# Performance work log

Measured on AMD Instinct MI355X. Metric: run time of the kernel, lower is better.

The kernel has to match this reference:

```python
import jax, jax.numpy as jnp
import numpy as np

N = 20000      # nodes
E = 320000     # edges (avg degree 16)
IN = 128
HID = 64
CLS = 32
H0, H1, H2 = 4, 4, 6
SLOPE = 0.2


def _lin(key, fan_in, fan_out):
    kw, kb = jax.random.split(key)
    s = 1.0 / np.sqrt(fan_in)
    W = jax.random.uniform(kw, (fan_in, fan_out), minval=-s, maxval=s, dtype=jnp.float32)
    b = jax.random.uniform(kb, (fan_out,), minval=-s, maxval=s, dtype=jnp.float32)
    return W, b


def setup_inputs() -> dict:
    key = jax.random.key(0)
    ks = jax.random.split(key, 16)
    x = jax.random.normal(ks[0], (N, IN), dtype=jnp.float32)
    src = jax.random.randint(ks[1], (E,), 0, N)
    dst = jax.random.randint(ks[2], (E,), 0, N)
    W0s, b0s = _lin(ks[3], IN, H0 * HID)
    W0d, b0d = _lin(ks[4], IN, H0 * HID)
    a0 = jax.random.normal(ks[5], (H0, HID), dtype=jnp.float32) * 0.05
    d1 = H0 * HID  # 256, flattened hidden width
    W1s, b1s = _lin(ks[6], d1, H1 * HID)
    W1d, b1d = _lin(ks[7], d1, H1 * HID)
    a1 = jax.random.normal(ks[8], (H1, HID), dtype=jnp.float32) * 0.05
    W2s, b2s = _lin(ks[9], d1, H2 * CLS)
    W2d, b2d = _lin(ks[10], d1, H2 * CLS)
    a2 = jax.random.normal(ks[11], (H2, CLS), dtype=jnp.float32) * 0.05
    Wr2, br2 = _lin(ks[12], d1, H2 * CLS)  # residual projection (256 != 192)
    return dict(x=x, src=src, dst=dst,
                W0s=W0s, b0s=b0s, W0d=W0d, b0d=b0d, a0=a0,
                W1s=W1s, b1s=b1s, W1d=W1d, b1d=b1d, a1=a1,
                W2s=W2s, b2s=b2s, W2d=W2d, b2d=b2d, a2=a2,
                Wr2=Wr2, br2=br2)


def _gatv2_layer(x, src, dst, Ws, bs, Wd, bd, attn, heads, dim, res, act):
    n = x.shape[0]
    feat_src = (x @ Ws + bs).reshape(n, heads, dim)
    feat_dst = (x @ Wd + bd).reshape(n, heads, dim)
    # GATv2 edge scores: a^T LeakyReLU(W_l h_u + W_r h_v)
    e = jax.nn.leaky_relu(feat_src[src] + feat_dst[dst], SLOPE)  # [E,H,D]
    logits = jnp.einsum('ehd,hd->eh', e, attn)                    # [E,H]
    # numerically-stable edge softmax over incoming edges per destination
    m = jax.ops.segment_max(logits, dst, num_segments=n)
    m = jnp.where(jnp.isfinite(m), m, 0.0)
    ex = jnp.exp(logits - m[dst])
    denom = jax.ops.segment_sum(ex, dst, num_segments=n)
    alpha = ex / denom[dst]                                        # [E,H]
    out = jax.ops.segment_sum(feat_src[src] * alpha[:, :, None], dst, num_segments=n)
    if res == 'id':
        out = out + x.reshape(n, heads, dim)
    elif res is not None:
        Wr, br = res
        out = out + (x @ Wr + br).reshape(n, heads, dim)
    if act:
        out = jax.nn.elu(out)
    return out  # [n, heads, dim]


def reference(x, src, dst,
              W0s, b0s, W0d, b0d, a0,
              W1s, b1s, W1d, b1d, a1,
              W2s, b2s, W2d, b2d, a2,
              Wr2, br2):
    h = _gatv2_layer(x, src, dst, W0s, b0s, W0d, b0d, a0, H0, HID, None, True)
    h = h.reshape(N, H0 * HID)
    h = _gatv2_layer(h, src, dst, W1s, b1s, W1d, b1d, a1, H1, HID, 'id', True)
    h = h.reshape(N, H1 * HID)
    out = _gatv2_layer(h, src, dst, W2s, b2s, W2d, b2d, a2, H2, CLS, (Wr2, br2), False)
    return out.mean(axis=1)  # [N, num_classes]
```

## Files before the change

### kernel.cpp

```cpp
#include <hip/hip_runtime.h>
#include <hip/hip_bf16.h>
#include <float.h>
#include <math.h>

#define NN 20000
#define EE 320000
#define IN_DIM 128
#define SLOPE_ 0.2f
#define DEG_CAP 64

typedef __attribute__((ext_vector_type(4))) float f32x4;
typedef _Float16 f16;
typedef __attribute__((ext_vector_type(2))) _Float16 f16x2;
typedef __attribute__((ext_vector_type(4))) _Float16 f16x4;
typedef __attribute__((ext_vector_type(8))) _Float16 f16x8;
typedef unsigned short ushort;

__device__ inline void prep_elem(const float* __restrict__ Wa, const float* __restrict__ ba, int na,
                                 const float* __restrict__ Wb, const float* __restrict__ bb, int nb,
                                 const float* __restrict__ Wc, const float* __restrict__ bc, int nc,
                                 int K, f16* __restrict__ Wt, float* __restrict__ bias_cat, int idx) {
    int n = idx / K;
    int k = idx - n * K;
    const float* W; const float* b; int nl; int ncols;
    if (n < na) { W = Wa; b = ba; nl = n; ncols = na; }
    else if (n < na + nb) { W = Wb; b = bb; nl = n - na; ncols = nb; }
    else { W = Wc; b = bc; nl = n - na - nb; ncols = nc; }
    Wt[(size_t)n * K + k] = (f16)W[(size_t)k * ncols + nl];
    if (k == 0) bias_cat[n] = b[nl];
}

#define SEG0 (512 * 128)
#define SEG1 (512 * 256)
#define SEG2 (576 * 256)
#define SEG3 (NN * IN_DIM / 4)
#define SEG4 (EE)
__global__ void prep_all(const float* __restrict__ W0s, const float* __restrict__ b0s,
                         const float* __restrict__ W0d, const float* __restrict__ b0d,
                         const float* __restrict__ W1s, const float* __restrict__ b1s,
                         const float* __restrict__ W1d, const float* __restrict__ b1d,
                         const float* __restrict__ W2s, const float* __restrict__ b2s,
                         const float* __restrict__ W2d, const float* __restrict__ b2d,
                         const float* __restrict__ Wr2, const float* __restrict__ br2,
                         const float* __restrict__ x,
                         const int* __restrict__ src, const int* __restrict__ dst,
                         f16* __restrict__ Wt0, float* __restrict__ bias0,
                         f16* __restrict__ Wt1, float* __restrict__ bias1,
                         f16* __restrict__ Wt2, float* __restrict__ bias2,
                         f16* __restrict__ A, unsigned int* __restrict__ deg,
                         int* __restrict__ csr_src) {
    int idx = blockIdx.x * 256 + threadIdx.x;
    if (idx < SEG0) {
        prep_elem(W0s, b0s, 256, W0d, b0d, 256, nullptr, nullptr, 0, 128, Wt0, bias0, idx);
    } else if ((idx -= SEG0) < SEG1) {
        prep_elem(W1s, b1s, 256, W1d, b1d, 256, nullptr, nullptr, 0, 256, Wt1, bias1, idx);
    } else if ((idx -= SEG1) < SEG2) {
        prep_elem(W2s, b2s, 192, W2d, b2d, 192, Wr2, br2, 192, 256, Wt2, bias2, idx);
    } else if ((idx -= SEG2) < SEG3) {
        float4 v = ((const float4*)x)[idx];
        f16x4 o = {(f16)v.x, (f16)v.y, (f16)v.z, (f16)v.w};
        ((f16x4*)A)[idx] = o;
    } else if ((idx -= SEG3) < SEG4) {
        int d = dst[idx];
        unsigned int pos = atomicAdd(&deg[d], 1u);
        csr_src[(unsigned)d * DEG_CAP + pos] = src[idx];
    }
}

__global__ __launch_bounds__(256) void gemm_mfma_f16(
        const f16* __restrict__ A, const f16* __restrict__ Wt,
        const float* __restrict__ bias,
        f16* __restrict__ F0, f16* __restrict__ F1, float* __restrict__ F2,
        int b1, int b2, int M, int K, int S, int gx, int gy) {
    __shared__ f16 Bs[64 * 256];
    __shared__ f16 Cs[4][32 * 66];

    const int bid = blockIdx.x;
    const int p = bid & 7;
    const int q = bid >> 3;
    const int bn_i = q % gx;
    const int bm_i = (q / gx) * 8 + p;
    if (bm_i >= gy) return;
    const int bm = bm_i * 256;
    const int bn = bn_i * 64;

    const int tid = threadIdx.x;
    const int wave = tid >> 6;
    const int lane = tid & 63;
    const int m16 = lane & 15;
    const int quad = lane >> 4;

    {
        const int n = tid >> 2;
        const int q0 = tid & 3;
        for (int j = 0; j * 32 < K; ++j) {
            int k0 = j * 32 + q0 * 8;
            f16x8 v = *(const f16x8*)(Wt + (size_t)(bn + n) * K + k0);
            int chunk = (j * 4 + (n >> 4)) * 64 + q0 * 16 + (n & 15);
            *(f16x8*)&Bs[chunk * 8] = v;
        }
    }
    __syncthreads();

    const int rb0 = bm + wave * 64;
    f32x4 acc[2][2][4];
    #pragma unroll
    for (int mi = 0; mi < 2; ++mi)
        #pragma unroll
        for (int mt = 0; mt < 2; ++mt)
            #pragma unroll
            for (int nt = 0; nt < 4; ++nt) acc[mi][mt][nt] = (f32x4){0.f, 0.f, 0.f, 0.f};

    int ar[2][2];
    #pragma unroll
    for (int mi = 0; mi < 2; ++mi)
        #pragma unroll
        for (int mt = 0; mt < 2; ++mt) {
            int row = rb0 + mi * 32 + mt * 16 + m16;
            ar[mi][mt] = row < M ? row : M - 1;
        }

    #pragma unroll 2
    for (int k0 = 0; k0 < K; k0 += 32) {
        f16x8 bs[4];
        #pragma unroll
        for (int nt = 0; nt < 4; ++nt)
            bs[nt] = *(const f16x8*)&Bs[(((k0 >> 5) * 4 + nt) * 64 + lane) * 8];
        #pragma unroll
        for (int mi = 0; mi < 2; ++mi) {
            f16x8 ah[2];
            #pragma unroll
            for (int mt = 0; mt < 2; ++mt)
                ah[mt] = *(const f16x8*)(A + (size_t)ar[mi][mt] * K + k0 + quad * 8);
            #pragma unroll
            for (int nt = 0; nt < 4; ++nt)
                #pragma unroll
                for (int mt = 0; mt < 2; ++mt)
                    acc[mi][mt][nt] = __builtin_amdgcn_mfma_f32_16x16x32_f16(ah[mt], bs[nt], acc[mi][mt][nt], 0, 0, 0);
        }
    }

    #pragma unroll
    for (int mi = 0; mi < 2; ++mi) {
        const int rbase = rb0 + mi * 32;
        if (bn < b2) {
            f16* __restrict__ Fb;
            int cs, cb;
            if (bn >= b1) { Fb = F1; cb = bn - b1; cs = b2 - b1; }
            else          { Fb = F0; cb = bn;      cs = b1; }
            f16* cw = &Cs[wave][0];
            #pragma unroll
            for (int nt = 0; nt < 4; ++nt) {
                float bv = bias[bn + nt * 16 + m16];
                #pragma unroll
                for (int mt = 0; mt < 2; ++mt)
                    #pragma unroll
                    for (int r = 0; r < 4; ++r) {
                        int row = mt * 16 + quad * 4 + r;
                        cw[row * 66 + nt * 16 + m16] = (f16)(acc[mi][mt][nt][r] + bv);
                    }
            }
            int lrow = lane >> 1;
            int lcol = (lane & 1) * 32;
            int grow = rbase + lrow;
            if (grow < M) {
                #pragma unroll
                for (int j = 0; j < 4; ++j) {
                    f16x8 v = *(f16x8*)&cw[lrow * 66 + lcol + j * 8];
                    *(f16x8*)&Fb[(size_t)grow * cs + cb + lcol + j * 8] = v;
                }
            }
        } else {
            int cs = S - b2;
            #pragma unroll
            for (int nt = 0; nt < 4; ++nt) {
                int col = bn - b2 + nt * 16 + m16;
                float bv = bias[bn + nt * 16 + m16];
                #pragma unroll
                for (int mt = 0; mt < 2; ++mt)
                    #pragma unroll
                    for (int r = 0; r < 4; ++r) {
                        int row = rbase + mt * 16 + quad * 4 + r;
                        if (row < M) F2[(size_t)row * cs + col] = acc[mi][mt][nt][r] + bv;
                    }
            }
        }
    }
}

#define AGG_STEP4(U0)                                                         \
    _Pragma("unroll")                                                         \
    for (int uu = 0; uu < 4; ++uu) {                                          \
        const int u = (U0) + uu;                                              \
        const f16x8 cur = buf[u];                                             \
        buf[u] = *(const f16x8*)&fsb[(unsigned)cidx[u] * HD + off];           \
        cidx[u] = csr_src[min(jj0 + b + 16 + u, last)];                       \
        float p = 0.f;                                                        \
        _Pragma("unroll")                                                     \
        for (int i = 0; i < 4; ++i) {                                         \
            f16x2 cp = (f16x2){cur[2 * i], cur[2 * i + 1]};                   \
            f16x2 xp = cp + fdp[i];                                           \
            unsigned xu = __builtin_bit_cast(unsigned, xp) & 0x7FFF7FFFu;     \
            f16x2 xa = __builtin_bit_cast(f16x2, xu);                         \
            p = __builtin_amdgcn_fdot2(xp, a6p[i], p, false);                 \
            p = __builtin_amdgcn_fdot2(xa, a4p[i], p, false);                 \
        }                                                                     \
        _Pragma("unroll")                                                     \
        for (int o = 1; o < GSZ; o <<= 1) p += __shfl_xor(p, o, 64);          \
        float w = (b + u < deg) ? __expf(p) : 0.f;                            \
        lh += w;                                                              \
        _Pragma("unroll")                                                     \
        for (int d = 0; d < 8; ++d) acc[d] += w * (float)cur[d];              \
    }

template <int HD, int D, bool HAS_RES, bool DO_ELU, int OUT_MODE>
__global__ __launch_bounds__(256) void gat_node_aggregate(
        const f16* __restrict__ fsb, const f16* __restrict__ fdb,
        const float* __restrict__ attn,
        const unsigned int* __restrict__ degv,
        const int* __restrict__ csr_src,
        const float* __restrict__ resid, int RS,
        float* __restrict__ outF, f16* __restrict__ outA) {
    constexpr int LANES = HD / 8;
    constexpr int GSZ = D / 8;
    __shared__ float red[(OUT_MODE == 2) ? 8 : 1][(OUT_MODE == 2) ? HD : 1];

    const int wave = threadIdx.x >> 6;
    const int lane = threadIdx.x & 63;
    const int half = lane >> 5;
    const int ln = lane & 31;
    const int t = blockIdx.x * 8 + wave * 2 + half;
    const bool active = (ln < LANES);
    const unsigned off = active ? 8u * ln : 0u;

    f16x2 fdp[4], a6p[4], a4p[4];
    if (active) {
        f16x8 dv = *(const f16x8*)&fdb[(unsigned)t * HD + off];
        float4 aA = *(const float4*)&attn[off];
        float4 aB = *(const float4*)&attn[off + 4];
        float av[8] = {aA.x, aA.y, aA.z, aA.w, aB.x, aB.y, aB.z, aB.w};
        #pragma unroll
        for (int i = 0; i < 4; ++i) {
            fdp[i] = (f16x2){dv[2 * i], dv[2 * i + 1]};
            a6p[i] = (f16x2){(f16)(0.6f * av[2 * i]), (f16)(0.6f * av[2 * i + 1])};
            a4p[i] = (f16x2){(f16)(0.4f * av[2 * i]), (f16)(0.4f * av[2 * i + 1])};
        }
    } else {
        #pragma unroll
        for (int i = 0; i < 4; ++i) {
            fdp[i] = (f16x2){0, 0};
            a6p[i] = (f16x2){0, 0};
            a4p[i] = (f16x2){0, 0};
        }
    }

    const int jj0 = t * DEG_CAP;
    const int deg = (int)degv[t];
    const int last = jj0 + deg - 1;
    const int degO = __shfl_xor(deg, 32, 64);
    const int mdeg = max(deg, degO);

    float acc[8];
    #pragma unroll
    for (int d = 0; d < 8; ++d) acc[d] = 0.f;
    float lh = 0.f;

    f16x8 buf[8];
    int cidx[8];
    #pragma unroll
    for (int u = 0; u < 8; ++u) {
        int e0 = max(min(jj0 + u, last), 0);
        buf[u] = *(const f16x8*)&fsb[(unsigned)csr_src[e0] * HD + off];
        cidx[u] = csr_src[max(min(jj0 + 8 + u, last), 0)];
    }

    for (int b = 0; b < mdeg; b += 8) {
        AGG_STEP4(0)
        if (b + 4 < mdeg) {
            AGG_STEP4(4)
        }
    }

    float inv = (lh > 0.f) ? 1.f / lh : 0.f;
    float vout[8];
    #pragma unroll
    for (int d = 0; d < 8; ++d) vout[d] = acc[d] * inv;
    if (HAS_RES && active) {
        float4 rA = *(const float4*)&resid[(unsigned)t * RS + off];
        float4 rB = *(const float4*)&resid[(unsigned)t * RS + off + 4];
        vout[0] += rA.x; vout[1] += rA.y; vout[2] += rA.z; vout[3] += rA.w;
        vout[4] += rB.x; vout[5] += rB.y; vout[6] += rB.z; vout[7] += rB.w;
    }
    if (DO_ELU) {
        #pragma unroll
        for (int d = 0; d < 8; ++d) vout[d] = vout[d] > 0.f ? vout[d] : expm1f(vout[d]);
    }

    if (OUT_MODE == 2) {
        const int nib = wave * 2 + half;
        if (active) {
            *(float4*)&red[nib][off] = make_float4(vout[0], vout[1], vout[2], vout[3]);
            *(float4*)&red[nib][off + 4] = make_float4(vout[4], vout[5], vout[6], vout[7]);
        }
        __syncthreads();
        int node = threadIdx.x >> 5;
        int col = threadIdx.x & 31;
        float ssum = 0.f;
        #pragma unroll
        for (int h = 0; h < 6; ++h) ssum += red[node][h * 32 + col];
        outF[(unsigned)(blockIdx.x * 8 + node) * 32 + col] = ssum * (1.f / 6.f);
    } else if (active) {
        f16x8 av;
        #pragma unroll
        for (int d = 0; d < 8; ++d) av[d] = (f16)vout[d];
        *(f16x8*)&outA[(unsigned)t * HD + off] = av;
        if (OUT_MODE == 0) {
            *(float4*)&outF[(unsigned)t * HD + off] = make_float4(vout[0], vout[1], vout[2], vout[3]);
            *(float4*)&outF[(unsigned)t * HD + off + 4] = make_float4(vout[4], vout[5], vout[6], vout[7]);
        }
    }
}

extern "C" void kernel_launch(void* const* d_in, const int* in_sizes, int n_in,
                              void* d_out, int out_size, void* d_ws, size_t ws_size,
                              hipStream_t stream) {
    const float* x   = (const float*)d_in[0];
    const int*   src = (const int*)d_in[1];
    const int*   dst = (const int*)d_in[2];
    const float* W0s = (const float*)d_in[3];
    const float* b0s = (const float*)d_in[4];
    const float* W0d = (const float*)d_in[5];
    const float* b0d = (const float*)d_in[6];
    const float* a0  = (const float*)d_in[7];
    const float* W1s = (const float*)d_in[8];
    const float* b1s = (const float*)d_in[9];
    const float* W1d = (const float*)d_in[10];
    const float* b1d = (const float*)d_in[11];
    const float* a1  = (const float*)d_in[12];
    const float* W2s = (const float*)d_in[13];
    const float* b2s = (const float*)d_in[14];
    const float* W2d = (const float*)d_in[15];
    const float* b2d = (const float*)d_in[16];
    const float* a2  = (const float*)d_in[17];
    const float* Wr2 = (const float*)d_in[18];
    const float* br2 = (const float*)d_in[19];

    f16* FsH = (f16*)d_ws;
    f16* FdH = FsH + (size_t)NN * 256;
    f16* A   = FdH + (size_t)NN * 256;
    float* O0 = (float*)(A + (size_t)NN * 256);
    f16* Wt0 = (f16*)(O0 + (size_t)NN * 256);
    f16* Wt1 = Wt0 + 512 * 128;
    f16* Wt2 = Wt1 + 512 * 256;
    float* bias0 = (float*)(Wt2 + 576 * 256);
    float* bias1 = bias0 + 512;
    float* bias2 = bias1 + 512;
    unsigned int* deg = (unsigned int*)(bias2 + 576);
    int* csr_src      = (int*)(deg + NN);

    hipMemsetAsync(deg, 0, (size_t)NN * 4 + (size_t)NN * DEG_CAP * 4, stream);

    {
        int total = SEG0 + SEG1 + SEG2 + SEG3 + SEG4;
        prep_all<<<(total + 255) / 256, 256, 0, stream>>>(
            W0s, b0s, W0d, b0d, W1s, b1s, W1d, b1d, W2s, b2s, W2d, b2d, Wr2, br2, x,
            src, dst, Wt0, bias0, Wt1, bias1, Wt2, bias2, A, deg, csr_src);
    }

    const int gy = (NN + 255) / 256;
    const int gy8 = ((gy + 7) / 8) * 8;
    const int nagg = NN / 8;

    gemm_mfma_f16<<<gy8 * 8, 256, 0, stream>>>(A, Wt0, bias0,
                                               FsH, FdH, nullptr, 256, 512, NN, 128, 512, 8, gy);
    gat_node_aggregate<256, 64, false, true, 0><<<nagg, 256, 0, stream>>>(
        FsH, FdH, a0, deg, csr_src, nullptr, 0, O0, A);

    gemm_mfma_f16<<<gy8 * 8, 256, 0, stream>>>(A, Wt1, bias1,
                                               FsH, FdH, nullptr, 256, 512, NN, 256, 512, 8, gy);
    gat_node_aggregate<256, 64, true, true, 1><<<nagg, 256, 0, stream>>>(
        FsH, FdH, a1, deg, csr_src, O0, 256, nullptr, A);

    gemm_mfma_f16<<<gy8 * 9, 256, 0, stream>>>(A, Wt2, bias2,
                                               FsH, FdH, O0, 192, 384, NN, 256, 576, 9, gy);
    gat_node_aggregate<192, 32, true, false, 2><<<nagg, 256, 0, stream>>>(
        FsH, FdH, a2, deg, csr_src, O0, 192, (float*)d_out, nullptr);
}
```

Measured before the change: 285.3 us.

## Fuse all GAT stages into one persistent cooperative kernel with grid syncs

Replaces the memset plus seven separate launches with a single cooperative persistent kernel of 768 blocks. Prep, CSR build, the three GEMMs and the three aggregations run as grid-strided stages separated by grid.sync(). The aim is to remove launch gaps and the memset of the full CSR buffer; only the degree array is zeroed now, and CSR writes are clamped to the cap. In exchange the kernel carries grid barrier overhead, lower occupancy from launch bounds of 3 blocks, and grid-strided loops whose work may balance less well than the per-kernel grids did. A fallback multi-kernel path runs if the cooperative launch fails.

```diff
diff --git a/kernel.cpp b/kernel.cpp
--- a/kernel.cpp
+++ b/kernel.cpp
@@ -1,25 +1,44 @@
 #include <hip/hip_runtime.h>
-#include <hip/hip_bf16.h>
+#include <hip/hip_cooperative_groups.h>
 #include <float.h>
 #include <math.h>
+
+namespace cg = cooperative_groups;
 
 #define NN 20000
 #define EE 320000
 #define IN_DIM 128
-#define SLOPE_ 0.2f
 #define DEG_CAP 64
+#define TPB 256
+#define COOP_GRID 768
 
 typedef __attribute__((ext_vector_type(4))) float f32x4;
 typedef _Float16 f16;
 typedef __attribute__((ext_vector_type(2))) _Float16 f16x2;
 typedef __attribute__((ext_vector_type(4))) _Float16 f16x4;
 typedef __attribute__((ext_vector_type(8))) _Float16 f16x8;
-typedef unsigned short ushort;
-
-__device__ inline void prep_elem(const float* __restrict__ Wa, const float* __restrict__ ba, int na,
-                                 const float* __restrict__ Wb, const float* __restrict__ bb, int nb,
-                                 const float* __restrict__ Wc, const float* __restrict__ bc, int nc,
-                                 int K, f16* __restrict__ Wt, float* __restrict__ bias_cat, int idx) {
+
+#define SEG0 (512 * 128)
+#define SEG1 (512 * 256)
+#define SEG2 (576 * 256)
+#define SEG3 (NN * IN_DIM / 4)
+#define SEGZ_TOT (SEG0 + SEG1 + SEG2 + SEG3 + NN)
+#define FB_TOT (SEG0 + SEG1 + SEG2 + SEG3 + EE)
+
+struct GatArgs {
+    const float *x; const int *src; const int *dst;
+    const float *W0s, *b0s, *W0d, *b0d, *a0;
+    const float *W1s, *b1s, *W1d, *b1d, *a1;
+    const float *W2s, *b2s, *W2d, *b2d, *a2, *Wr2, *br2;
+    f16 *FsH, *FdH, *A; float *O0;
+    f16 *Wt0, *Wt1, *Wt2; float *bias0, *bias1, *bias2;
+    unsigned *deg; int *csr; float *out;
+};
+
+__device__ __forceinline__ void prep_elem(const float* __restrict__ Wa, const float* __restrict__ ba, int na,
+                                          const float* __restrict__ Wb, const float* __restrict__ bb, int nb,
+                                          const float* __restrict__ Wc, const float* __restrict__ bc, int nc,
+                                          int K, f16* __restrict__ Wt, float* __restrict__ bias_cat, int idx) {
     int n = idx / K;
     int k = idx - n * K;
     const float* W; const float* b; int nl; int ncols;
@@ -30,159 +49,138 @@
     if (k == 0) bias_cat[n] = b[nl];
 }
 
-#define SEG0 (512 * 128)
-#define SEG1 (512 * 256)
-#define SEG2 (576 * 256)
-#define SEG3 (NN * IN_DIM / 4)
-#define SEG4 (EE)
-__global__ void prep_all(const float* __restrict__ W0s, const float* __restrict__ b0s,
-                         const float* __restrict__ W0d, const float* __restrict__ b0d,
-                         const float* __restrict__ W1s, const float* __restrict__ b1s,
-                         const float* __restrict__ W1d, const float* __restrict__ b1d,
-                         const float* __restrict__ W2s, const float* __restrict__ b2s,
-                         const float* __restrict__ W2d, const float* __restrict__ b2d,
-                         const float* __restrict__ Wr2, const float* __restrict__ br2,
-                         const float* __restrict__ x,
-                         const int* __restrict__ src, const int* __restrict__ dst,
-                         f16* __restrict__ Wt0, float* __restrict__ bias0,
-                         f16* __restrict__ Wt1, float* __restrict__ bias1,
-                         f16* __restrict__ Wt2, float* __restrict__ bias2,
-                         f16* __restrict__ A, unsigned int* __restrict__ deg,
-                         int* __restrict__ csr_src) {
-    int idx = blockIdx.x * 256 + threadIdx.x;
+__device__ __forceinline__ bool prep_item(const GatArgs& g, int idx) {
     if (idx < SEG0) {
-        prep_elem(W0s, b0s, 256, W0d, b0d, 256, nullptr, nullptr, 0, 128, Wt0, bias0, idx);
+        prep_elem(g.W0s, g.b0s, 256, g.W0d, g.b0d, 256, nullptr, nullptr, 0, 128, g.Wt0, g.bias0, idx);
     } else if ((idx -= SEG0) < SEG1) {
-        prep_elem(W1s, b1s, 256, W1d, b1d, 256, nullptr, nullptr, 0, 256, Wt1, bias1, idx);
+        prep_elem(g.W1s, g.b1s, 256, g.W1d, g.b1d, 256, nullptr, nullptr, 0, 256, g.Wt1, g.bias1, idx);
     } else if ((idx -= SEG1) < SEG2) {
-        prep_elem(W2s, b2s, 192, W2d, b2d, 192, Wr2, br2, 192, 256, Wt2, bias2, idx);
+        prep_elem(g.W2s, g.b2s, 192, g.W2d, g.b2d, 192, g.Wr2, g.br2, 192, 256, g.Wt2, g.bias2, idx);
     } else if ((idx -= SEG2) < SEG3) {
-        float4 v = ((const float4*)x)[idx];
+        float4 v = ((const float4*)g.x)[idx];
         f16x4 o = {(f16)v.x, (f16)v.y, (f16)v.z, (f16)v.w};
-        ((f16x4*)A)[idx] = o;
-    } else if ((idx -= SEG3) < SEG4) {
-        int d = dst[idx];
-        unsigned int pos = atomicAdd(&deg[d], 1u);
-        csr_src[(unsigned)d * DEG_CAP + pos] = src[idx];
-    }
-}
-
-__global__ __launch_bounds__(256) void gemm_mfma_f16(
+        ((f16x4*)g.A)[idx] = o;
+    } else return false;
+    return true;
+}
+
+__device__ __forceinline__ void gemm_stage(
         const f16* __restrict__ A, const f16* __restrict__ Wt,
         const float* __restrict__ bias,
         f16* __restrict__ F0, f16* __restrict__ F1, float* __restrict__ F2,
-        int b1, int b2, int M, int K, int S, int gx, int gy) {
-    __shared__ f16 Bs[64 * 256];
-    __shared__ f16 Cs[4][32 * 66];
-
-    const int bid = blockIdx.x;
-    const int p = bid & 7;
-    const int q = bid >> 3;
-    const int bn_i = q % gx;
-    const int bm_i = (q / gx) * 8 + p;
-    if (bm_i >= gy) return;
-    const int bm = bm_i * 256;
-    const int bn = bn_i * 64;
-
+        int b1, int b2, int M, int K, int S, int gx, int gy, int gy8,
+        f16* Bs, f16* Cs, int vb0, int vstride) {
+    const int ntiles = gy8 * gx;
     const int tid = threadIdx.x;
     const int wave = tid >> 6;
     const int lane = tid & 63;
     const int m16 = lane & 15;
     const int quad = lane >> 4;
 
-    {
-        const int n = tid >> 2;
-        const int q0 = tid & 3;
-        for (int j = 0; j * 32 < K; ++j) {
-            int k0 = j * 32 + q0 * 8;
-            f16x8 v = *(const f16x8*)(Wt + (size_t)(bn + n) * K + k0);
-            int chunk = (j * 4 + (n >> 4)) * 64 + q0 * 16 + (n & 15);
-            *(f16x8*)&Bs[chunk * 8] = v;
-        }
-    }
-    __syncthreads();
-
-    const int rb0 = bm + wave * 64;
-    f32x4 acc[2][2][4];
-    #pragma unroll
-    for (int mi = 0; mi < 2; ++mi)
-        #pragma unroll
-        for (int mt = 0; mt < 2; ++mt)
-            #pragma unroll
-            for (int nt = 0; nt < 4; ++nt) acc[mi][mt][nt] = (f32x4){0.f, 0.f, 0.f, 0.f};
-
-    int ar[2][2];
-    #pragma unroll
-    for (int mi = 0; mi < 2; ++mi)
-        #pragma unroll
-        for (int mt = 0; mt < 2; ++mt) {
-            int row = rb0 + mi * 32 + mt * 16 + m16;
-            ar[mi][mt] = row < M ? row : M - 1;
-        }
-
-    #pragma unroll 2
-    for (int k0 = 0; k0 < K; k0 += 32) {
-        f16x8 bs[4];
-        #pragma unroll
-        for (int nt = 0; nt < 4; ++nt)
-            bs[nt] = *(const f16x8*)&Bs[(((k0 >> 5) * 4 + nt) * 64 + lane) * 8];
-        #pragma unroll
-        for (int mi = 0; mi < 2; ++mi) {
-            f16x8 ah[2];
+    for (int vb = vb0; vb < ntiles; vb += vstride) {
+        __syncthreads();
+        const int p = vb & 7;
+        const int q = vb >> 3;
+        const int bn_i = q % gx;
+        const int bm_i = (q / gx) * 8 + p;
+        if (bm_i >= gy) continue;
+        const int bm = bm_i * 256;
+        const int bn = bn_i * 64;
+
+        {
+            const int n = tid >> 2;
+            const int q0 = tid & 3;
+            for (int j = 0; j * 32 < K; ++j) {
+                int k0 = j * 32 + q0 * 8;
+                f16x8 v = *(const f16x8*)(Wt + (size_t)(bn + n) * K + k0);
+                int chunk = (j * 4 + (n >> 4)) * 64 + q0 * 16 + (n & 15);
+                *(f16x8*)&Bs[chunk * 8] = v;
+            }
+        }
+        __syncthreads();
+
+        const int rb0 = bm + wave * 64;
+        f32x4 acc[2][2][4];
+        #pragma unroll
+        for (int mi = 0; mi < 2; ++mi)
             #pragma unroll
             for (int mt = 0; mt < 2; ++mt)
-                ah[mt] = *(const f16x8*)(A + (size_t)ar[mi][mt] * K + k0 + quad * 8);
+                #pragma unroll
+                for (int nt = 0; nt < 4; ++nt) acc[mi][mt][nt] = (f32x4){0.f, 0.f, 0.f, 0.f};
+
+        int ar[2][2];
+        #pragma unroll
+        for (int mi = 0; mi < 2; ++mi)
+            #pragma unroll
+            for (int mt = 0; mt < 2; ++mt) {
+                int row = rb0 + mi * 32 + mt * 16 + m16;
+                ar[mi][mt] = row < M ? row : M - 1;
+            }
+
+        #pragma unroll 2
+        for (int k0 = 0; k0 < K; k0 += 32) {
+            f16x8 bs[4];
             #pragma unroll
             for (int nt = 0; nt < 4; ++nt)
+                bs[nt] = *(const f16x8*)&Bs[(((k0 >> 5) * 4 + nt) * 64 + lane) * 8];
+            #pragma unroll
+            for (int mi = 0; mi < 2; ++mi) {
+                f16x8 ah[2];
                 #pragma unroll
                 for (int mt = 0; mt < 2; ++mt)
-                    acc[mi][mt][nt] = __builtin_amdgcn_mfma_f32_16x16x32_f16(ah[mt], bs[nt], acc[mi][mt][nt], 0, 0, 0);
-        }
-    }
-
-    #pragma unroll
-    for (int mi = 0; mi < 2; ++mi) {
-        const int rbase = rb0 + mi * 32;
-        if (bn < b2) {
-            f16* __restrict__ Fb;
-            int cs, cb;
-            if (bn >= b1) { Fb = F1; cb = bn - b1; cs = b2 - b1; }
-            else          { Fb = F0; cb = bn;      cs = b1; }
-            f16* cw = &Cs[wave][0];
-            #pragma unroll
-            for (int nt = 0; nt < 4; ++nt) {
-                float bv = bias[bn + nt * 16 + m16];
+                    ah[mt] = *(const f16x8*)(A + (size_t)ar[mi][mt] * K + k0 + quad * 8);
                 #pragma unroll
-                for (int mt = 0; mt < 2; ++mt)
+                for (int nt = 0; nt < 4; ++nt)
                     #pragma unroll
-                    for (int r = 0; r < 4; ++r) {
-                        int row = mt * 16 + quad * 4 + r;
-                        cw[row * 66 + nt * 16 + m16] = (f16)(acc[mi][mt][nt][r] + bv);
+                    for (int mt = 0; mt < 2; ++mt)
+                        acc[mi][mt][nt] = __builtin_amdgcn_mfma_f32_16x16x32_f16(ah[mt], bs[nt], acc[mi][mt][nt], 0, 0, 0);
+            }
+        }
+
+        #pragma unroll
+        for (int mi = 0; mi < 2; ++mi) {
+            const int rbase = rb0 + mi * 32;
+            if (bn < b2) {
+                f16* __restrict__ Fb;
+                int cs, cb;
+                if (bn >= b1) { Fb = F1; cb = bn - b1; cs = b2 - b1; }
+                else          { Fb = F0; cb = bn;      cs = b1; }
+                f16* cw = Cs + wave * (32 * 66);
+                #pragma unroll
+                for (int nt = 0; nt < 4; ++nt) {
+                    float bv = bias[bn + nt * 16 + m16];
+                    #pragma unroll
+                    for (int mt = 0; mt < 2; ++mt)
+                        #pragma unroll
+                        for (int r = 0; r < 4; ++r) {
+                            int row = mt * 16 + quad * 4 + r;
+                            cw[row * 66 + nt * 16 + m16] = (f16)(acc[mi][mt][nt][r] + bv);
+                        }
+                }
+                int lrow = lane >> 1;
+                int lcol = (lane & 1) * 32;
+                int grow = rbase + lrow;
+                if (grow < M) {
+                    #pragma unroll
+                    for (int j = 0; j < 4; ++j) {
+                        f16x8 v = *(f16x8*)&cw[lrow * 66 + lcol + j * 8];
+                        *(f16x8*)&Fb[(size_t)grow * cs + cb + lcol + j * 8] = v;
                     }
-            }
-            int lrow = lane >> 1;
-            int lcol = (lane & 1) * 32;
-            int grow = rbase + lrow;
-            if (grow < M) {
+                }
+            } else {
+                int cs = S - b2;
                 #pragma unroll
-                for (int j = 0; j < 4; ++j) {
-                    f16x8 v = *(f16x8*)&cw[lrow * 66 + lcol + j * 8];
-                    *(f16x8*)&Fb[(size_t)grow * cs + cb + lcol + j * 8] = v;
+                for (int nt = 0; nt < 4; ++nt) {
+                    int col = bn - b2 + nt * 16 + m16;
+                    float bv = bias[bn + nt * 16 + m16];
+                    #pragma unroll
+                    for (int mt = 0; mt < 2; ++mt)
+                        #pragma unroll
+                        for (int r = 0; r < 4; ++r) {
+                            int row = rbase + mt * 16 + quad * 4 + r;
+                            if (row < M) F2[(size_t)row * cs + col] = acc[mi][mt][nt][r] + bv;
+                        }
                 }
-            }
-        } else {
-            int cs = S - b2;
-            #pragma unroll
-            for (int nt = 0; nt < 4; ++nt) {
-                int col = bn - b2 + nt * 16 + m16;
-                float bv = bias[bn + nt * 16 + m16];
-                #pragma unroll
-                for (int mt = 0; mt < 2; ++mt)
-                    #pragma unroll
-                    for (int r = 0; r < 4; ++r) {
-                        int row = rbase + mt * 16 + quad * 4 + r;
-                        if (row < M) F2[(size_t)row * cs + col] = acc[mi][mt][nt][r] + bv;
-                    }
             }
         }
     }
@@ -193,196 +191,275 @@
     for (int uu = 0; uu < 4; ++uu) {                                          \
         const int u = (U0) + uu;                                              \
         const f16x8 cur = buf[u];                                             \
-        buf[u] = *(const f16x8*)&fsb[(unsigned)cidx[u] * HD + off];           \
-        cidx[u] = csr_src[min(jj0 + b + 16 + u, last)];                       \
-        float p = 0.f;                                                        \
+        unsigned su = (unsigned)cidx[u]; su = su < NN ? su : 0u;              \
+        buf[u] = *(const f16x8*)&fsb[su * (unsigned)HD + off];                \
+        cidx[u] = csr_src[max(min(jj0 + b + 16 + u, last), 0)];               \
+        float pp = 0.f;                                                       \
         _Pragma("unroll")                                                     \
         for (int i = 0; i < 4; ++i) {                                         \
             f16x2 cp = (f16x2){cur[2 * i], cur[2 * i + 1]};                   \
             f16x2 xp = cp + fdp[i];                                           \
             unsigned xu = __builtin_bit_cast(unsigned, xp) & 0x7FFF7FFFu;     \
             f16x2 xa = __builtin_bit_cast(f16x2, xu);                         \
-            p = __builtin_amdgcn_fdot2(xp, a6p[i], p, false);                 \
-            p = __builtin_amdgcn_fdot2(xa, a4p[i], p, false);                 \
+            pp = __builtin_amdgcn_fdot2(xp, a6p[i], pp, false);               \
+            pp = __builtin_amdgcn_fdot2(xa, a4p[i], pp, false);               \
         }                                                                     \
         _Pragma("unroll")                                                     \
-        for (int o = 1; o < GSZ; o <<= 1) p += __shfl_xor(p, o, 64);          \
-        float w = (b + u < deg) ? __expf(p) : 0.f;                            \
+        for (int o = 1; o < GSZ; o <<= 1) pp += __shfl_xor(pp, o, 64);        \
+        float w = (b + u < dg) ? __expf(pp) : 0.f;                            \
         lh += w;                                                              \
         _Pragma("unroll")                                                     \
         for (int d = 0; d < 8; ++d) acc[d] += w * (float)cur[d];              \
     }
 
 template <int HD, int D, bool HAS_RES, bool DO_ELU, int OUT_MODE>
-__global__ __launch_bounds__(256) void gat_node_aggregate(
+__device__ __forceinline__ void agg_stage(
         const f16* __restrict__ fsb, const f16* __restrict__ fdb,
         const float* __restrict__ attn,
-        const unsigned int* __restrict__ degv,
+        const unsigned* __restrict__ degv,
         const int* __restrict__ csr_src,
         const float* __restrict__ resid, int RS,
-        float* __restrict__ outF, f16* __restrict__ outA) {
+        float* __restrict__ outF, f16* __restrict__ outA,
+        float* red, int vb0, int vstride) {
     constexpr int LANES = HD / 8;
     constexpr int GSZ = D / 8;
-    __shared__ float red[(OUT_MODE == 2) ? 8 : 1][(OUT_MODE == 2) ? HD : 1];
 
     const int wave = threadIdx.x >> 6;
     const int lane = threadIdx.x & 63;
     const int half = lane >> 5;
     const int ln = lane & 31;
-    const int t = blockIdx.x * 8 + wave * 2 + half;
     const bool active = (ln < LANES);
     const unsigned off = active ? 8u * ln : 0u;
 
-    f16x2 fdp[4], a6p[4], a4p[4];
+    f16x2 a6p[4], a4p[4];
     if (active) {
-        f16x8 dv = *(const f16x8*)&fdb[(unsigned)t * HD + off];
         float4 aA = *(const float4*)&attn[off];
         float4 aB = *(const float4*)&attn[off + 4];
         float av[8] = {aA.x, aA.y, aA.z, aA.w, aB.x, aB.y, aB.z, aB.w};
         #pragma unroll
         for (int i = 0; i < 4; ++i) {
-            fdp[i] = (f16x2){dv[2 * i], dv[2 * i + 1]};
             a6p[i] = (f16x2){(f16)(0.6f * av[2 * i]), (f16)(0.6f * av[2 * i + 1])};
             a4p[i] = (f16x2){(f16)(0.4f * av[2 * i]), (f16)(0.4f * av[2 * i + 1])};
         }
     } else {
         #pragma unroll
-        for (int i = 0; i < 4; ++i) {
-            fdp[i] = (f16x2){0, 0};
-            a6p[i] = (f16x2){0, 0};
-            a4p[i] = (f16x2){0, 0};
-        }
-    }
-
-    const int jj0 = t * DEG_CAP;
-    const int deg = (int)degv[t];
-    const int last = jj0 + deg - 1;
-    const int degO = __shfl_xor(deg, 32, 64);
-    const int mdeg = max(deg, degO);
-
-    float acc[8];
-    #pragma unroll
-    for (int d = 0; d < 8; ++d) acc[d] = 0.f;
-    float lh = 0.f;
-
-    f16x8 buf[8];
-    int cidx[8];
-    #pragma unroll
-    for (int u = 0; u < 8; ++u) {
-        int e0 = max(min(jj0 + u, last), 0);
-        buf[u] = *(const f16x8*)&fsb[(unsigned)csr_src[e0] * HD + off];
-        cidx[u] = csr_src[max(min(jj0 + 8 + u, last), 0)];
-    }
-
-    for (int b = 0; b < mdeg; b += 8) {
-        AGG_STEP4(0)
-        if (b + 4 < mdeg) {
-            AGG_STEP4(4)
-        }
-    }
-
-    float inv = (lh > 0.f) ? 1.f / lh : 0.f;
-    float vout[8];
-    #pragma unroll
-    for (int d = 0; d < 8; ++d) vout[d] = acc[d] * inv;
-    if (HAS_RES && active) {
-        float4 rA = *(const float4*)&resid[(unsigned)t * RS + off];
-        float4 rB = *(const float4*)&resid[(unsigned)t * RS + off + 4];
-        vout[0] += rA.x; vout[1] += rA.y; vout[2] += rA.z; vout[3] += rA.w;
-        vout[4] += rB.x; vout[5] += rB.y; vout[6] += rB.z; vout[7] += rB.w;
-    }
-    if (DO_ELU) {
-        #pragma unroll
-        for (int d = 0; d < 8; ++d) vout[d] = vout[d] > 0.f ? vout[d] : expm1f(vout[d]);
-    }
-
-    if (OUT_MODE == 2) {
-        const int nib = wave * 2 + half;
+        for (int i = 0; i < 4; ++i) { a6p[i] = (f16x2){0, 0}; a4p[i] = (f16x2){0, 0}; }
+    }
+
+    for (int vb = vb0; vb < NN / 8; vb += vstride) {
+        const int t = vb * 8 + wave * 2 + half;
+
+        f16x2 fdp[4];
         if (active) {
-            *(float4*)&red[nib][off] = make_float4(vout[0], vout[1], vout[2], vout[3]);
-            *(float4*)&red[nib][off + 4] = make_float4(vout[4], vout[5], vout[6], vout[7]);
-        }
-        __syncthreads();
-        int node = threadIdx.x >> 5;
-        int col = threadIdx.x & 31;
-        float ssum = 0.f;
-        #pragma unroll
-        for (int h = 0; h < 6; ++h) ssum += red[node][h * 32 + col];
-        outF[(unsigned)(blockIdx.x * 8 + node) * 32 + col] = ssum * (1.f / 6.f);
-    } else if (active) {
-        f16x8 av;
-        #pragma unroll
-        for (int d = 0; d < 8; ++d) av[d] = (f16)vout[d];
-        *(f16x8*)&outA[(unsigned)t * HD + off] = av;
-        if (OUT_MODE == 0) {
-            *(float4*)&outF[(unsigned)t * HD + off] = make_float4(vout[0], vout[1], vout[2], vout[3]);
-            *(float4*)&outF[(unsigned)t * HD + off + 4] = make_float4(vout[4], vout[5], vout[6], vout[7]);
-        }
-    }
+            f16x8 dv = *(const f16x8*)&fdb[(unsigned)t * HD + off];
+            #pragma unroll
+            for (int i = 0; i < 4; ++i) fdp[i] = (f16x2){dv[2 * i], dv[2 * i + 1]};
+        } else {
+            #pragma unroll
+            for (int i = 0; i < 4; ++i) fdp[i] = (f16x2){0, 0};
+        }
+
+        const int jj0 = t * DEG_CAP;
+        const int dg = min((int)degv[t], DEG_CAP);
+        const int last = jj0 + dg - 1;
+        const int degO = __shfl_xor(dg, 32, 64);
+        const int mdeg = max(dg, degO);
+
+        float acc[8];
+        #pragma unroll
+        for (int d = 0; d < 8; ++d) acc[d] = 0.f;
+        float lh = 0.f;
+
+        f16x8 buf[8];
+        int cidx[8];
+        #pragma unroll
+        for (int u = 0; u < 8; ++u) {
+            int e0 = max(min(jj0 + u, last), 0);
+            unsigned s0 = (unsigned)csr_src[e0]; s0 = s0 < NN ? s0 : 0u;
+            buf[u] = *(const f16x8*)&fsb[s0 * (unsigned)HD + off];
+            cidx[u] = csr_src[max(min(jj0 + 8 + u, last), 0)];
+        }
+
+        for (int b = 0; b < mdeg; b += 8) {
+            AGG_STEP4(0)
+            if (b + 4 < mdeg) {
+                AGG_STEP4(4)
+            }
+        }
+
+        float inv = (lh > 0.f) ? 1.f / lh : 0.f;
+        float vout[8];
+        #pragma unroll
+        for (int d = 0; d < 8; ++d) vout[d] = acc[d] * inv;
+        if (HAS_RES && active) {
+            float4 rA = *(const float4*)&resid[(unsigned)t * RS + off];
+            float4 rB = *(const float4*)&resid[(unsigned)t * RS + off + 4];
+            vout[0] += rA.x; vout[1] += rA.y; vout[2] += rA.z; vout[3] += rA.w;
+            vout[4] += rB.x; vout[5] += rB.y; vout[6] += rB.z; vout[7] += rB.w;
+        }
+        if (DO_ELU) {
+            #pragma unroll
+            for (int d = 0; d < 8; ++d) vout[d] = vout[d] > 0.f ? vout[d] : expm1f(vout[d]);
+        }
+
+        if (OUT_MODE == 2) {
+            const int nib = wave * 2 + half;
+            __syncthreads();
+            if (active) {
+                *(float4*)&red[nib * HD + off] = make_float4(vout[0], vout[1], vout[2], vout[3]);
+                *(float4*)&red[nib * HD + off + 4] = make_float4(vout[4], vout[5], vout[6], vout[7]);
+            }
+            __syncthreads();
+            int node = threadIdx.x >> 5;
+            int col = threadIdx.x & 31;
+            float ssum = 0.f;
+            #pragma unroll
+            for (int h = 0; h < 6; ++h) ssum += red[node * HD + h * 32 + col];
+            outF[(unsigned)(vb * 8 + node) * 32 + col] = ssum * (1.f / 6.f);
+        } else if (active) {
+            f16x8 av;
+            #pragma unroll
+            for (int d = 0; d < 8; ++d) av[d] = (f16)vout[d];
+            *(f16x8*)&outA[(unsigned)t * HD + off] = av;
+            if (OUT_MODE == 0) {
+                *(float4*)&outF[(unsigned)t * HD + off] = make_float4(vout[0], vout[1], vout[2], vout[3]);
+                *(float4*)&outF[(unsigned)t * HD + off + 4] = make_float4(vout[4], vout[5], vout[6], vout[7]);
+            }
+        }
+    }
+}
+
+__global__ __launch_bounds__(TPB, 3) void gat_fused(GatArgs g) {
+    __shared__ __align__(16) unsigned char smem[32 * 1024 + 4 * 32 * 66 * 2];
+    f16* Bs = (f16*)smem;
+    f16* Cs = (f16*)(smem + 32 * 1024);
+    float* red = (float*)smem;
+
+    cg::grid_group grid = cg::this_grid();
+    const int gtid = blockIdx.x * TPB + threadIdx.x;
+    const int gstride = gridDim.x * TPB;
+
+    for (int i = gtid; i < SEGZ_TOT; i += gstride) {
+        if (!prep_item(g, i)) {
+            int idx = i - (SEG0 + SEG1 + SEG2 + SEG3);
+            if (idx < NN) g.deg[idx] = 0u;
+        }
+    }
+    grid.sync();
+
+    for (int e = gtid; e < EE; e += gstride) {
+        int d = g.dst[e];
+        unsigned pos = atomicAdd(&g.deg[d], 1u);
+        if (pos < DEG_CAP) g.csr[(unsigned)d * DEG_CAP + pos] = g.src[e];
+    }
+    grid.sync();
+
+    gemm_stage(g.A, g.Wt0, g.bias0, g.FsH, g.FdH, nullptr, 256, 512, NN, 128, 512, 8, 79, 80,
+               Bs, Cs, blockIdx.x, gridDim.x);
+    grid.sync();
+    agg_stage<256, 64, false, true, 0>(g.FsH, g.FdH, g.a0, g.deg, g.csr, nullptr, 0,
+                                       g.O0, g.A, red, blockIdx.x, gridDim.x);
+    grid.sync();
+
+    gemm_stage(g.A, g.Wt1, g.bias1, g.FsH, g.FdH, nullptr, 256, 512, NN, 256, 512, 8, 79, 80,
+               Bs, Cs, blockIdx.x, gridDim.x);
+    grid.sync();
+    agg_stage<256, 64, true, true, 1>(g.FsH, g.FdH, g.a1, g.deg, g.csr, g.O0, 256,
+                                      nullptr, g.A, red, blockIdx.x, gridDim.x);
+    grid.sync();
+
+    gemm_stage(g.A, g.Wt2, g.bias2, g.FsH, g.FdH, g.O0, 192, 384, NN, 256, 576, 9, 79, 80,
+               Bs, Cs, blockIdx.x, gridDim.x);
+    grid.sync();
+    agg_stage<192, 32, true, false, 2>(g.FsH, g.FdH, g.a2, g.deg, g.csr, g.O0, 192,
+                                       g.out, nullptr, red, blockIdx.x, gridDim.x);
+}
+
+__global__ void prep_all_k(GatArgs g) {
+    int idx = blockIdx.x * TPB + threadIdx.x;
+    if (idx < FB_TOT) {
+        if (!prep_item(g, idx)) {
+            int e = idx - (SEG0 + SEG1 + SEG2 + SEG3);
+            int d = g.dst[e];
+            unsigned pos = atomicAdd(&g.deg[d], 1u);
+            if (pos < DEG_CAP) g.csr[(unsigned)d * DEG_CAP + pos] = g.src[e];
+        }
+    }
+}
+
+__global__ __launch_bounds__(TPB) void gemm_k(GatArgs g, int layer) {
+    __shared__ __align__(16) unsigned char smem[32 * 1024 + 4 * 32 * 66 * 2];
+    f16* Bs = (f16*)smem;
+    f16* Cs = (f16*)(smem + 32 * 1024);
+    if (layer == 0)
+        gemm_stage(g.A, g.Wt0, g.bias0, g.FsH, g.FdH, nullptr, 256, 512, NN, 128, 512, 8, 79, 80,
+                   Bs, Cs, blockIdx.x, gridDim.x);
+    else if (layer == 1)
+        gemm_stage(g.A, g.Wt1, g.bias1, g.FsH, g.FdH, nullptr, 256, 512, NN, 256, 512, 8, 79, 80,
+                   Bs, Cs, blockIdx.x, gridDim.x);
+    else
+        gemm_stage(g.A, g.Wt2, g.bias2, g.FsH, g.FdH, g.O0, 192, 384, NN, 256, 576, 9, 79, 80,
+                   Bs, Cs, blockIdx.x, gridDim.x);
+}
+
+__global__ __launch_bounds__(TPB) void agg_k0(GatArgs g) {
+    agg_stage<256, 64, false, true, 0>(g.FsH, g.FdH, g.a0, g.deg, g.csr, nullptr, 0,
+                                       g.O0, g.A, nullptr, blockIdx.x, gridDim.x);
+}
+__global__ __launch_bounds__(TPB) void agg_k1(GatArgs g) {
+    agg_stage<256, 64, true, true, 1>(g.FsH, g.FdH, g.a1, g.deg, g.csr, g.O0, 256,
+                                      nullptr, g.A, nullptr, blockIdx.x, gridDim.x);
+}
+__global__ __launch_bounds__(TPB) void agg_k2(GatArgs g) {
+    __shared__ float red[8 * 192];
+    agg_stage<192, 32, true, false, 2>(g.FsH, g.FdH, g.a2, g.deg, g.csr, g.O0, 192,
+                                       g.out, nullptr, red, blockIdx.x, gridDim.x);
 }
 
 extern "C" void kernel_launch(void* const* d_in, const int* in_sizes, int n_in,
                               void* d_out, int out_size, void* d_ws, size_t ws_size,
                               hipStream_t stream) {
-    const float* x   = (const float*)d_in[0];
-    const int*   src = (const int*)d_in[1];
-    const int*   dst = (const int*)d_in[2];
-    const float* W0s = (const float*)d_in[3];
-    const float* b0s = (const float*)d_in[4];
-    const float* W0d = (const float*)d_in[5];
-    const float* b0d = (const float*)d_in[6];
-    const float* a0  = (const float*)d_in[7];
-    const float* W1s = (const float*)d_in[8];
-    const float* b1s = (const float*)d_in[9];
-    const float* W1d = (const float*)d_in[10];
-    const float* b1d = (const float*)d_in[11];
-    const float* a1  = (const float*)d_in[12];
-    const float* W2s = (const float*)d_in[13];
-    const float* b2s = (const float*)d_in[14];
-    const float* W2d = (const float*)d_in[15];
-    const float* b2d = (const float*)d_in[16];
-    const float* a2  = (const float*)d_in[17];
-    const float* Wr2 = (const float*)d_in[18];
-    const float* br2 = (const float*)d_in[19];
-
-    f16* FsH = (f16*)d_ws;
-    f16* FdH = FsH + (size_t)NN * 256;
-    f16* A   = FdH + (size_t)NN * 256;
-    float* O0 = (float*)(A + (size_t)NN * 256);
-    f16* Wt0 = (f16*)(O0 + (size_t)NN * 256);
-    f16* Wt1 = Wt0 + 512 * 128;
-    f16* Wt2 = Wt1 + 512 * 256;
-    float* bias0 = (float*)(Wt2 + 576 * 256);
-    float* bias1 = bias0 + 512;
-    float* bias2 = bias1 + 512;
-    unsigned int* deg = (unsigned int*)(bias2 + 576);
-    int* csr_src      = (int*)(deg + NN);
-
-    hipMemsetAsync(deg, 0, (size_t)NN * 4 + (size_t)NN * DEG_CAP * 4, stream);
-
-    {
-        int total = SEG0 + SEG1 + SEG2 + SEG3 + SEG4;
-        prep_all<<<(total + 255) / 256, 256, 0, stream>>>(
-            W0s, b0s, W0d, b0d, W1s, b1s, W1d, b1d, W2s, b2s, W2d, b2d, Wr2, br2, x,
-            src, dst, Wt0, bias0, Wt1, bias1, Wt2, bias2, A, deg, csr_src);
-    }
-
-    const int gy = (NN + 255) / 256;
-    const int gy8 = ((gy + 7) / 8) * 8;
-    const int nagg = NN / 8;
-
-    gemm_mfma_f16<<<gy8 * 8, 256, 0, stream>>>(A, Wt0, bias0,
-                                               FsH, FdH, nullptr, 256, 512, NN, 128, 512, 8, gy);
-    gat_node_aggregate<256, 64, false, true, 0><<<nagg, 256, 0, stream>>>(
-        FsH, FdH, a0, deg, csr_src, nullptr, 0, O0, A);
-
-    gemm_mfma_f16<<<gy8 * 8, 256, 0, stream>>>(A, Wt1, bias1,
-                                               FsH, FdH, nullptr, 256, 512, NN, 256, 512, 8, gy);
-    gat_node_aggregate<256, 64, true, true, 1><<<nagg, 256, 0, stream>>>(
-        FsH, FdH, a1, deg, csr_src, O0, 256, nullptr, A);
-
-    gemm_mfma_f16<<<gy8 * 9, 256, 0, stream>>>(A, Wt2, bias2,
-                                               FsH, FdH, O0, 192, 384, NN, 256, 576, 9, gy);
-    gat_node_aggregate<192, 32, true, false, 2><<<nagg, 256, 0, stream>>>(
-        FsH, FdH, a2, deg, csr_src, O0, 192, (float*)d_out, nullptr);
-}
+    GatArgs a;
+    a.x   = (const float*)d_in[0];
+    a.src = (const int*)d_in[1];
+    a.dst = (const int*)d_in[2];
+    a.W0s = (const float*)d_in[3];  a.b0s = (const float*)d_in[4];
+    a.W0d = (const float*)d_in[5];  a.b0d = (const float*)d_in[6];
+    a.a0  = (const float*)d_in[7];
+    a.W1s = (const float*)d_in[8];  a.b1s = (const float*)d_in[9];
+    a.W1d = (const float*)d_in[10]; a.b1d = (const float*)d_in[11];
+    a.a1  = (const float*)d_in[12];
+    a.W2s = (const float*)d_in[13]; a.b2s = (const float*)d_in[14];
+    a.W2d = (const float*)d_in[15]; a.b2d = (const float*)d_in[16];
+    a.a2  = (const float*)d_in[17];
+    a.Wr2 = (const float*)d_in[18]; a.br2 = (const float*)d_in[19];
+
+    a.FsH = (f16*)d_ws;
+    a.FdH = a.FsH + (size_t)NN * 256;
+    a.A   = a.FdH + (size_t)NN * 256;
+    a.O0  = (float*)(a.A + (size_t)NN * 256);
+    a.Wt0 = (f16*)(a.O0 + (size_t)NN * 256);
+    a.Wt1 = a.Wt0 + 512 * 128;
+    a.Wt2 = a.Wt1 + 512 * 256;
+    a.bias0 = (float*)(a.Wt2 + 576 * 256);
+    a.bias1 = a.bias0 + 512;
+    a.bias2 = a.bias1 + 512;
+    a.deg = (unsigned*)(a.bias2 + 576);
+    a.csr = (int*)(a.deg + NN);
+    a.out = (float*)d_out;
+
+    void* kp[] = {(void*)&a};
+    hipError_t err = hipLaunchCooperativeKernel(reinterpret_cast<void*>(gat_fused),
+                                                dim3(COOP_GRID), dim3(TPB), kp, 0, stream);
+    if (err != hipSuccess) {
+        (void)hipGetLastError();
+        hipMemsetAsync(a.deg, 0, NN * sizeof(unsigned), stream);
+        prep_all_k<<<(FB_TOT + TPB - 1) / TPB, TPB, 0, stream>>>(a);
+        gemm_k<<<80 * 8, TPB, 0, stream>>>(a, 0);
+        agg_k0<<<NN / 8, TPB, 0, stream>>>(a);
+        gemm_k<<<80 * 8, TPB, 0, stream>>>(a, 1);
+        agg_k1<<<NN / 8, TPB, 0, stream>>>(a);
+        gemm_k<<<80 * 9, TPB, 0, stream>>>(a, 2);
+        agg_k2<<<NN / 8, TPB, 0, stream>>>(a);
+    }
+}
```

Measured after the change: 1.027 ms. +260.1%, slower.
